# Optimization experiments

Measured on AMD Instinct MI355X. Metric: run time of the kernel, lower is better.

## Reference

```python
import jax, jax.numpy as jnp
import numpy as np

STRIDE = 2
PAD = 1
DIL = 1
OUTPAD = 0

def _depthwise_deconv(x, w):
    """Depthwise ConvTranspose2d. x: [B, G, H, W], w: [G, 1, kh, kw]."""
    g = x.shape[1]
    kh, kw = w.shape[-2], w.shape[-1]
    ph = (DIL * (kh - 1) - PAD, DIL * (kh - 1) - PAD + OUTPAD)
    pw = (DIL * (kw - 1) - PAD, DIL * (kw - 1) - PAD + OUTPAD)
    w_f = w[:, :, ::-1, ::-1]  # spatial flip for transpose conv
    return jax.lax.conv_general_dilated(
        x, w_f, window_strides=(1, 1), padding=[ph, pw],
        lhs_dilation=(STRIDE, STRIDE), rhs_dilation=(DIL, DIL),
        dimension_numbers=('NCHW', 'OIHW', 'NCHW'),
        feature_group_count=g)


def setup_inputs() -> dict:
    key = jax.random.key(0)
    k1, k2, k3 = jax.random.split(key, 3)
    B, C, H, W = 2, 32, 96, 96
    O, KH, KW = 48, 4, 4
    x = jax.random.normal(k1, (B, C, H, W), dtype=jnp.float32)
    # positive weights keep the ones-normalizer strictly positive
    weight = jax.random.uniform(k2, (O, C, KH, KW), dtype=jnp.float32)
    bias = jax.random.normal(k3, (O,), dtype=jnp.float32)
    return {"x": x, "weight": weight, "bias": bias}


def reference(x, weight, bias):
    B, C, H, W = x.shape
    O = weight.shape[0]
    kh, kw = weight.shape[2], weight.shape[3]
    # Stack all O depthwise deconvs into one grouped deconv over O*C channels.
    w = weight.reshape(O * C, 1, kh, kw)
    xr = jnp.tile(x, (1, O, 1, 1))                      # [B, O*C, H, W]
    y = _depthwise_deconv(xr, w)                        # [B, O*C, Ho, Wo]
    ones = jnp.ones((1, O * C, H, W), dtype=x.dtype)
    norm = _depthwise_deconv(ones, w)                   # [1, O*C, Ho, Wo]
    Ho, Wo = y.shape[2], y.shape[3]
    out = (y / norm).reshape(B, O, C, Ho, Wo).sum(axis=2)  # sum over in_channels
    return out + bias[None, :, None, None]
```

## Files before the change

kernel.cpp:

```cpp
#include <hip/hip_runtime.h>

#define C_IN  32
#define O_OUT 48
#define H_IN  96
#define W_IN  96
#define H_OUT 192
#define W_OUT 192
#define HW_IN (H_IN * W_IN)
#define NCBLK 192
#define NFBLK 16
#define LPAD  40
#define XS_BYTES (3 * 100 * LPAD * 2)
#define WOS   516

typedef __attribute__((ext_vector_type(8))) short bf16x8;
typedef __attribute__((ext_vector_type(4))) float f32x4;

__device__ __forceinline__ unsigned short f2bf(float f) {
    union { float f; unsigned u; } v; v.f = f;
    unsigned u = v.u + 0x7FFFu + ((v.u >> 16) & 1u);
    return (unsigned short)(u >> 16);
}

__global__ __launch_bounds__(768) void nct_all(
    const float* __restrict__ x,
    const float* __restrict__ weight,
    const float* __restrict__ bias,
    float* __restrict__ out)
{
    __shared__ __align__(16) unsigned char smem[XS_BYTES + O_OUT * WOS * 4];
    const int blk = blockIdx.x;
    const int tid = threadIdx.x;

    if (blk < NCBLK) {
        auto xs = (unsigned short (*)[100][LPAD])smem;
        float* wl = (float*)(smem + XS_BYTES);

        const int b   = blk / 96;
        const int row = blk % 96;

        const int r3[3] = { (row > 0) ? row - 1 : 0, row, (row < H_IN - 1) ? row + 1 : H_IN - 1 };

        if (tid < 576) {
            const int r   = tid / 192;
            const int rem = tid - r * 192;
            const int pp  = rem >> 2;
            const int cg  = rem & 3;
            const int col = 2 * pp;
            const float* src = x + (size_t)(b * C_IN + cg * 8) * HW_IN + r3[r] * W_IN + col;
            float v0[8], v1[8];
            #pragma unroll
            for (int k = 0; k < 8; ++k) {
                const float2 v = *(const float2*)(src + (size_t)k * HW_IN);
                v0[k] = v.x; v1[k] = v.y;
            }
            unsigned p0[4], p1[4];
            #pragma unroll
            for (int k = 0; k < 4; ++k) {
                p0[k] = (unsigned)f2bf(v0[2 * k]) | ((unsigned)f2bf(v0[2 * k + 1]) << 16);
                p1[k] = (unsigned)f2bf(v1[2 * k]) | ((unsigned)f2bf(v1[2 * k + 1]) << 16);
            }
            *(uint4*)(&xs[r][col + 1][cg * 8]) = make_uint4(p0[0], p0[1], p0[2], p0[3]);
            *(uint4*)(&xs[r][col + 2][cg * 8]) = make_uint4(p1[0], p1[1], p1[2], p1[3]);
        } else if (tid < 600) {
            const int h    = tid - 576;
            const int r    = h >> 3;
            const int hs   = (h >> 2) & 1;
            const int cg   = h & 3;
            const int colx = hs ? 95 : 0;
            const int pix  = hs ? 97 : 0;
            const float* src = x + (size_t)(b * C_IN + cg * 8) * HW_IN + r3[r] * W_IN + colx;
            unsigned pk[4];
            #pragma unroll
            for (int k = 0; k < 4; ++k) {
                const float f0 = src[(size_t)(2 * k)     * HW_IN];
                const float f1 = src[(size_t)(2 * k + 1) * HW_IN];
                pk[k] = (unsigned)f2bf(f0) | ((unsigned)f2bf(f1) << 16);
            }
            *(uint4*)(&xs[r][pix][cg * 8]) = make_uint4(pk[0], pk[1], pk[2], pk[3]);
        }

        {
            const float4* wsrc = (const float4*)weight;
            #pragma unroll
            for (int k = 0; k < 8; ++k) {
                const int f = tid + k * 768;
                const int o = f >> 7;
                const int m = f & 127;
                const float4 v = wsrc[f];
                *(float4*)(wl + o * WOS + m * 4) = v;
            }
        }

        const int lane = tid & 63;
        const int wid  = tid >> 6;
        const int half = wid / 6;
        const int sub  = wid % 6;
        const int pe = sub & 1, mt = sub >> 1;
        const int g = lane >> 4, n16 = lane & 15;
        const int c0 = half * 48;

        const float4 bv4 = *(const float4*)(bias + mt * 16 + 4 * g);

        __syncthreads();

        const bool etop = (pe == 0 && row == 0);
        const bool ebot = (pe == 1 && row == H_IN - 1);
        const float m0 = ebot ? 0.f : 1.f;
        const float m1 = etop ? 0.f : 1.f;

        const int o = mt * 16 + n16;
        const float* wb0 = wl + o * WOS + g * 128 + (pe ? 0 : 4);
        const float* wb1 = wl + o * WOS + g * 128 + (pe ? 8 : 12);

        bf16x8 A[2][4];
        #pragma unroll
        for (int cc = 0; cc < 8; ++cc) {
            const float4 wa0 = *(const float4*)(wb0 + cc * 16);
            const float4 wa1 = *(const float4*)(wb1 + cc * 16);

            const float r0 = 1.f / (m0 * (wa0.y + wa0.w) + m1 * (wa1.y + wa1.w));
            const float r1 = 1.f / (m0 * (wa0.x + wa0.z) + m1 * (wa1.x + wa1.z));

            A[0][0][cc] = (short)f2bf(m0 * wa0.y * r0);
            A[0][1][cc] = (short)f2bf(m0 * wa0.w * r0);
            A[0][2][cc] = (short)f2bf(m1 * wa1.y * r0);
            A[0][3][cc] = (short)f2bf(m1 * wa1.w * r0);
            A[1][0][cc] = (short)f2bf(m0 * wa0.x * r1);
            A[1][1][cc] = (short)f2bf(m0 * wa0.z * r1);
            A[1][2][cc] = (short)f2bf(m1 * wa1.x * r1);
            A[1][3][cc] = (short)f2bf(m1 * wa1.z * r1);
        }

        const int lr0 = pe ? 2 : 1;
        const int lr1 = pe ? 1 : 0;
        const int ho  = 2 * row + pe;

        #pragma unroll
        for (int nt = 0; nt < 3; ++nt) {
            const int col = c0 + nt * 16 + n16;
            const int lp  = col + 1;

            const bf16x8 B00 = *(const bf16x8*)(&xs[lr0][lp][g * 8]);
            const bf16x8 B0m = *(const bf16x8*)(&xs[lr0][lp - 1][g * 8]);
            const bf16x8 B0p = *(const bf16x8*)(&xs[lr0][lp + 1][g * 8]);
            const bf16x8 B10 = *(const bf16x8*)(&xs[lr1][lp][g * 8]);
            const bf16x8 B1m = *(const bf16x8*)(&xs[lr1][lp - 1][g * 8]);
            const bf16x8 B1p = *(const bf16x8*)(&xs[lr1][lp + 1][g * 8]);

            f32x4 a0 = {0.f, 0.f, 0.f, 0.f}, a1 = {0.f, 0.f, 0.f, 0.f};
            a0 = __builtin_amdgcn_mfma_f32_16x16x32_bf16(A[0][0], B00, a0, 0, 0, 0);
            a0 = __builtin_amdgcn_mfma_f32_16x16x32_bf16(A[0][1], B0m, a0, 0, 0, 0);
            a0 = __builtin_amdgcn_mfma_f32_16x16x32_bf16(A[0][2], B10, a0, 0, 0, 0);
            a0 = __builtin_amdgcn_mfma_f32_16x16x32_bf16(A[0][3], B1m, a0, 0, 0, 0);
            a1 = __builtin_amdgcn_mfma_f32_16x16x32_bf16(A[1][0], B0p, a1, 0, 0, 0);
            a1 = __builtin_amdgcn_mfma_f32_16x16x32_bf16(A[1][1], B00, a1, 0, 0, 0);
            a1 = __builtin_amdgcn_mfma_f32_16x16x32_bf16(A[1][2], B1p, a1, 0, 0, 0);
            a1 = __builtin_amdgcn_mfma_f32_16x16x32_bf16(A[1][3], B10, a1, 0, 0, 0);

            #pragma unroll
            for (int r = 0; r < 4; ++r) {
                const int oo = mt * 16 + 4 * g + r;
                const float v0 = a0[r] + bv4[r];
                const float v1 = a1[r] + bv4[r];
                float* p = out + ((size_t)(b * O_OUT + oo) * H_OUT + ho) * W_OUT + 2 * col;
                if (col == 0)             p[1] = v1;
                else if (col == W_IN - 1) p[0] = v0;
                else                      *(float2*)p = make_float2(v0, v1);
            }
        }
    } else {
        float* xcol = (float*)smem;

        const int fb   = blk - NCBLK;
        const int b    = fb >> 3;
        const int side = (fb >> 2) & 1;
        const int og   = fb & 3;
        const int colx = side ? 95 : 0;

        for (int idx = tid; idx < C_IN * H_IN; idx += 768) {
            const int c = idx / H_IN;
            const int r = idx - c * H_IN;
            xcol[c * H_IN + r] = x[(size_t)(b * C_IN + c) * HW_IN + r * W_IN + colx];
        }
        __syncthreads();

        if (tid < 384) {
            const int o_loc  = tid >> 5;
            const int ho_loc = tid & 31;
            const int o      = og * 12 + o_loc;
            const int wo     = side ? 191 : 0;
            const int pe     = ho_loc & 1;
            const int jstar  = side ? 2 : 1;

            int   rA[6], rB[6];
            float mBf[6];
            #pragma unroll
            for (int k = 0; k < 6; ++k) {
                const int ho = ho_loc + 32 * k;
                const int s  = ho >> 1;
                rA[k] = s;
                if (pe) { const bool m = (s + 1 < H_IN); rB[k] = m ? s + 1 : H_IN - 1; mBf[k] = m ? 1.f : 0.f; }
                else    { const bool m = (s > 0);        rB[k] = m ? s - 1 : 0;        mBf[k] = m ? 1.f : 0.f; }
            }

            const int iA = pe ? 8 : 4;
            const int iB = pe ? 0 : 12;

            float acc[6] = {0.f, 0.f, 0.f, 0.f, 0.f, 0.f};
            const float* wb = weight + (size_t)o * (C_IN * 16);

            for (int c = 0; c < C_IN; ++c) {
                const float wA = wb[c * 16 + iA + jstar];
                const float wB = wb[c * 16 + iB + jstar];
                const float rn_int  = __builtin_amdgcn_rcpf(wA + wB);
                const float rn_edge = __builtin_amdgcn_rcpf(wA);
                const float* xc = xcol + c * H_IN;
                #pragma unroll
                for (int k = 0; k < 6; ++k) {
                    const float xA = xc[rA[k]];
                    const float xB = xc[rB[k]];
                    const float rn = (mBf[k] != 0.f) ? rn_int : rn_edge;
                    acc[k] += (wA * xA + mBf[k] * (wB * xB)) * rn;
                }
            }

            const float bv = bias[o];
            #pragma unroll
            for (int k = 0; k < 6; ++k) {
                const int ho = ho_loc + 32 * k;
                out[((size_t)(b * O_OUT + o) * H_OUT + ho) * W_OUT + wo] = acc[k] + bv;
            }
        }
    }
}

extern "C" void kernel_launch(void* const* d_in, const int* in_sizes, int n_in,
                              void* d_out, int out_size, void* d_ws, size_t ws_size,
                              hipStream_t stream) {
    const float* x    = (const float*)d_in[0];
    const float* w    = (const float*)d_in[1];
    const float* bias = (const float*)d_in[2];
    float* out = (float*)d_out;

    dim3 b768(768, 1, 1);
    dim3 gm(NCBLK + NFBLK, 1, 1);
    hipLaunchKernelGGL(nct_all, gm, b768, 0, stream, x, w, bias, out);
}
```

Measured before the change: 19.10 us.

## Stage MFMA outputs in shared memory for coalesced float4 stores; widen input loads

The interior blocks now write their MFMA results into an LDS buffer that reuses the weight region. After a barrier, all threads write the two output rows to global memory as contiguous float4 stores, replacing the scattered float2 stores. The input staging now uses float4 loads covering four columns per thread, with half as many threads doing the work. This adds two block barriers and extra LDS traffic in exchange for better global store and load coalescing.

```diff
diff --git a/kernel.cpp b/kernel.cpp
--- a/kernel.cpp
+++ b/kernel.cpp
@@ -12,6 +12,8 @@
 #define LPAD  40
 #define XS_BYTES (3 * 100 * LPAD * 2)
 #define WOS   516
+#define CSTR  196
+#define CPL   (O_OUT * CSTR)
 
 typedef __attribute__((ext_vector_type(8))) short bf16x8;
 typedef __attribute__((ext_vector_type(4))) float f32x4;
@@ -34,36 +36,42 @@
 
     if (blk < NCBLK) {
         auto xs = (unsigned short (*)[100][LPAD])smem;
-        float* wl = (float*)(smem + XS_BYTES);
+        float* wl   = (float*)(smem + XS_BYTES);
+        float* cbuf = (float*)(smem + XS_BYTES);
 
         const int b   = blk / 96;
         const int row = blk % 96;
 
         const int r3[3] = { (row > 0) ? row - 1 : 0, row, (row < H_IN - 1) ? row + 1 : H_IN - 1 };
 
-        if (tid < 576) {
-            const int r   = tid / 192;
-            const int rem = tid - r * 192;
-            const int pp  = rem >> 2;
+        if (tid < 288) {
+            const int r   = tid / 96;
+            const int rem = tid - r * 96;
+            const int q   = rem >> 2;
             const int cg  = rem & 3;
-            const int col = 2 * pp;
-            const float* src = x + (size_t)(b * C_IN + cg * 8) * HW_IN + r3[r] * W_IN + col;
-            float v0[8], v1[8];
-            #pragma unroll
-            for (int k = 0; k < 8; ++k) {
-                const float2 v = *(const float2*)(src + (size_t)k * HW_IN);
-                v0[k] = v.x; v1[k] = v.y;
-            }
-            unsigned p0[4], p1[4];
-            #pragma unroll
-            for (int k = 0; k < 4; ++k) {
-                p0[k] = (unsigned)f2bf(v0[2 * k]) | ((unsigned)f2bf(v0[2 * k + 1]) << 16);
-                p1[k] = (unsigned)f2bf(v1[2 * k]) | ((unsigned)f2bf(v1[2 * k + 1]) << 16);
-            }
-            *(uint4*)(&xs[r][col + 1][cg * 8]) = make_uint4(p0[0], p0[1], p0[2], p0[3]);
-            *(uint4*)(&xs[r][col + 2][cg * 8]) = make_uint4(p1[0], p1[1], p1[2], p1[3]);
-        } else if (tid < 600) {
-            const int h    = tid - 576;
+            const int col0 = q * 4;
+            const float* src = x + (size_t)(b * C_IN + cg * 8) * HW_IN + r3[r] * W_IN + col0;
+            float4 v[8];
+            #pragma unroll
+            for (int k = 0; k < 8; ++k) v[k] = *(const float4*)(src + (size_t)k * HW_IN);
+            #pragma unroll
+            for (int j = 0; j < 4; ++j) {
+                const float vj[8] = { j==0?v[0].x:j==1?v[0].y:j==2?v[0].z:v[0].w,
+                                      j==0?v[1].x:j==1?v[1].y:j==2?v[1].z:v[1].w,
+                                      j==0?v[2].x:j==1?v[2].y:j==2?v[2].z:v[2].w,
+                                      j==0?v[3].x:j==1?v[3].y:j==2?v[3].z:v[3].w,
+                                      j==0?v[4].x:j==1?v[4].y:j==2?v[4].z:v[4].w,
+                                      j==0?v[5].x:j==1?v[5].y:j==2?v[5].z:v[5].w,
+                                      j==0?v[6].x:j==1?v[6].y:j==2?v[6].z:v[6].w,
+                                      j==0?v[7].x:j==1?v[7].y:j==2?v[7].z:v[7].w };
+                unsigned pk[4];
+                #pragma unroll
+                for (int m = 0; m < 4; ++m)
+                    pk[m] = (unsigned)f2bf(vj[2 * m]) | ((unsigned)f2bf(vj[2 * m + 1]) << 16);
+                *(uint4*)(&xs[r][col0 + j + 1][cg * 8]) = make_uint4(pk[0], pk[1], pk[2], pk[3]);
+            }
+        } else if (tid < 312) {
+            const int h    = tid - 288;
             const int r    = h >> 3;
             const int hs   = (h >> 2) & 1;
             const int cg   = h & 3;
@@ -132,9 +140,10 @@
             A[1][3][cc] = (short)f2bf(m1 * wa1.z * r1);
         }
 
+        __syncthreads();
+
         const int lr0 = pe ? 2 : 1;
         const int lr1 = pe ? 1 : 0;
-        const int ho  = 2 * row + pe;
 
         #pragma unroll
         for (int nt = 0; nt < 3; ++nt) {
@@ -161,12 +170,33 @@
             #pragma unroll
             for (int r = 0; r < 4; ++r) {
                 const int oo = mt * 16 + 4 * g + r;
-                const float v0 = a0[r] + bv4[r];
-                const float v1 = a1[r] + bv4[r];
-                float* p = out + ((size_t)(b * O_OUT + oo) * H_OUT + ho) * W_OUT + 2 * col;
-                if (col == 0)             p[1] = v1;
-                else if (col == W_IN - 1) p[0] = v0;
-                else                      *(float2*)p = make_float2(v0, v1);
+                float* cp = cbuf + pe * CPL + oo * CSTR + 2 * col;
+                cp[0] = a0[r] + bv4[r];
+                cp[1] = a1[r] + bv4[r];
+            }
+        }
+
+        __syncthreads();
+
+        const int ho0 = 2 * row;
+        #pragma unroll
+        for (int k = 0; k < 6; ++k) {
+            const int j   = tid + k * 768;
+            const int pej = j / 2304;
+            const int rem = j - pej * 2304;
+            const int oo  = rem / 48;
+            const int wv  = rem - oo * 48;
+            const int wo0 = wv * 4;
+            const float4 v = *(const float4*)(cbuf + pej * CPL + oo * CSTR + wo0);
+            float* p = out + ((size_t)(b * O_OUT + oo) * H_OUT + ho0 + pej) * W_OUT + wo0;
+            if (wv == 0) {
+                p[1] = v.y;
+                *(float2*)(p + 2) = make_float2(v.z, v.w);
+            } else if (wv == 47) {
+                *(float2*)(p) = make_float2(v.x, v.y);
+                p[2] = v.z;
+            } else {
+                *(float4*)p = v;
             }
         }
     } else {
```

Result: slower. 19.65 us (+2.9%).
